# Performance work log

Measured on AMD Instinct MI355X. Metric: run time of the kernel, lower is better.

The kernel has to match this reference:

```python
import jax, jax.numpy as jnp
import numpy as np

N_USERS = 100000
N_ITEMS = 50000
N_NODES = N_USERS + N_ITEMS
EMB = 64
N_LAYERS = 3
N_EDGES = 4800000
AVG_DEG = 32


def setup_inputs() -> dict:
    key = jax.random.key(0)
    k1, k2, k3, k4, k5 = jax.random.split(key, 5)
    user_emb = jax.random.normal(k1, (N_USERS, EMB), dtype=jnp.float32) * 0.01
    item_emb = jax.random.normal(k2, (N_ITEMS, EMB), dtype=jnp.float32) * 0.01
    # normalized adjacency values ~ 1/deg
    adj_val = jax.random.uniform(k3, (N_EDGES,), dtype=jnp.float32) * (1.0 / AVG_DEG)
    adj_row = jax.random.randint(k4, (N_EDGES,), 0, N_NODES, dtype=jnp.int32)
    adj_col = jax.random.randint(k5, (N_EDGES,), 0, N_NODES, dtype=jnp.int32)
    return {"user_emb": user_emb, "item_emb": item_emb,
            "adj_val": adj_val, "adj_row": adj_row, "adj_col": adj_col}


def reference(user_emb, item_emb, adj_val, adj_row, adj_col):
    ego = jnp.concatenate([user_emb, item_emb], axis=0)  # [N_NODES, EMB]

    def spmm(x):
        # sparse_adj @ x via gather + segment-sum over destination rows
        msgs = adj_val[:, None] * x[adj_col]              # [N_EDGES, EMB]
        return jax.ops.segment_sum(msgs, adj_row, num_segments=N_NODES)

    acc = ego  # running sum for layer-mean (avoids stacking all layers)
    x = ego
    for _ in range(N_LAYERS):
        x = jax.nn.relu(spmm(x))
        acc = acc + x
    all_emb = acc / (N_LAYERS + 1)
    return all_emb[:N_USERS], all_emb[N_USERS:]
```

## Files before the change

### kernel.cpp

```cpp
#include <hip/hip_runtime.h>

#define N_USERS 100000
#define N_ITEMS 50000
#define N_NODES 150000
#define EMB 64
#define N_EDGES 4800000
#define N_LAYERS 3

#define RPB 128
#define NB 1172
#define MAXB 5120
#define CHUNK 8192
#define NCHUNKS ((N_EDGES + CHUNK - 1) / CHUNK)

__global__ __launch_bounds__(256) void init_kernel(
        const float2* __restrict__ user, const float2* __restrict__ item,
        unsigned short* __restrict__ x8, float* __restrict__ xs,
        float2* __restrict__ out) {
    int t = threadIdx.x;
    int p = t & 31;
    int r = blockIdx.x * 8 + (t >> 5);
    if (r >= N_NODES) return;
    float2 e = (r < N_USERS) ? user[r * 32 + p] : item[(r - N_USERS) * 32 + p];
    int o = r * 32 + p;
    out[o] = make_float2(0.25f * e.x, 0.25f * e.y);
    float m = fmaxf(fabsf(e.x), fabsf(e.y));
    #pragma unroll
    for (int mask = 16; mask; mask >>= 1) m = fmaxf(m, __shfl_xor(m, mask));
    float inv = (m > 0.f) ? 127.0f / m : 0.f;
    int q0 = (int)rintf(e.x * inv);
    int q1 = (int)rintf(e.y * inv);
    x8[o] = (unsigned short)((q0 & 0xFF) | ((q1 & 0xFF) << 8));
    if (p == 0) xs[r] = m * (1.0f / 127.0f);
}

__global__ __launch_bounds__(256) void hist_kernel(
        const int* __restrict__ row, int* __restrict__ counts) {
    __shared__ int h[NB];
    for (int i = threadIdx.x; i < NB; i += 256) h[i] = 0;
    __syncthreads();
    for (int i = blockIdx.x * 256 + threadIdx.x; i < N_EDGES; i += gridDim.x * 256)
        atomicAdd(&h[row[i] >> 7], 1);
    __syncthreads();
    for (int i = threadIdx.x; i < NB; i += 256) {
        int v = h[i];
        if (v) atomicAdd(&counts[i], v);
    }
}

__global__ __launch_bounds__(1024) void scan_kernel(
        const int* __restrict__ counts,
        int* __restrict__ bucketStart, int* __restrict__ cursor) {
    __shared__ int tmp[1024];
    int t = threadIdx.x;
    int i0 = 2 * t, i1 = 2 * t + 1;
    int v0 = (i0 < NB) ? counts[i0] : 0;
    int v1 = (i1 < NB) ? counts[i1] : 0;
    int s = v0 + v1;
    tmp[t] = s;
    __syncthreads();
    for (int off = 1; off < 1024; off <<= 1) {
        int u = (t >= off) ? tmp[t - off] : 0;
        __syncthreads();
        tmp[t] += u;
        __syncthreads();
    }
    int excl = tmp[t] - s;
    if (i0 < NB) { bucketStart[i0] = excl;      cursor[i0] = excl; }
    if (i1 < NB) { bucketStart[i1] = excl + v0; cursor[i1] = excl + v0; }
    if (t == 0) bucketStart[NB] = N_EDGES;
}

__global__ __launch_bounds__(512) void chunkscatter_kernel(
        const int* __restrict__ row, const int* __restrict__ col,
        const float* __restrict__ val,
        int* __restrict__ cursor, int2* __restrict__ sEdge) {
    __shared__ int2 rec[CHUNK];
    __shared__ unsigned short bidS[CHUNK];
    __shared__ int cnt[NB];
    __shared__ int lofs[NB];
    __shared__ int gbase[NB];
    __shared__ int tmp[512];

    int t = threadIdx.x;
    int e0 = blockIdx.x * CHUNK;
    int n = N_EDGES - e0; if (n > CHUNK) n = CHUNK;

    for (int i = t; i < NB; i += 512) cnt[i] = 0;
    __syncthreads();

    int2 myrec[16];
    int  myb[16];
    #pragma unroll
    for (int j = 0; j < 16; ++j) {
        int i = j * 512 + t;
        if (i < n) {
            int gi = e0 + i;
            int r = row[gi];
            int b = r >> 7;
            myrec[j] = make_int2(((r & (RPB - 1)) << 18) | col[gi],
                                 __float_as_int(val[gi]));
            myb[j] = b;
            atomicAdd(&cnt[b], 1);
        } else myb[j] = -1;
    }
    __syncthreads();

    int b3 = t * 3;
    int c0 = (b3     < NB) ? cnt[b3]     : 0;
    int c1 = (b3 + 1 < NB) ? cnt[b3 + 1] : 0;
    int c2 = (b3 + 2 < NB) ? cnt[b3 + 2] : 0;
    int s = c0 + c1 + c2;
    tmp[t] = s;
    __syncthreads();
    for (int off = 1; off < 512; off <<= 1) {
        int u = (t >= off) ? tmp[t - off] : 0;
        __syncthreads();
        tmp[t] += u;
        __syncthreads();
    }
    int excl = tmp[t] - s;
    if (b3     < NB) lofs[b3]     = excl;
    if (b3 + 1 < NB) lofs[b3 + 1] = excl + c0;
    if (b3 + 2 < NB) lofs[b3 + 2] = excl + c0 + c1;
    __syncthreads();

    for (int i = t; i < NB; i += 512) {
        int c = cnt[i];
        gbase[i] = c ? atomicAdd(&cursor[i], c) : 0;
        cnt[i] = lofs[i];
    }
    __syncthreads();

    #pragma unroll
    for (int j = 0; j < 16; ++j) {
        if (myb[j] >= 0) {
            int p = atomicAdd(&cnt[myb[j]], 1);
            rec[p] = myrec[j];
            bidS[p] = (unsigned short)myb[j];
        }
    }
    __syncthreads();

    for (int i = t; i < n; i += 512) {
        int b = bidS[i];
        sEdge[gbase[b] + (i - lofs[b])] = rec[i];
    }
}

__global__ __launch_bounds__(256) void localsort_kernel(
        const int* __restrict__ bucketStart, int2* __restrict__ sEdge,
        int* __restrict__ rowStart) {
    __shared__ int2 sorted[MAXB];
    __shared__ int lh[RPB];
    __shared__ int lsc[RPB];
    __shared__ int lcur[RPB];
    int b = blockIdx.x, t = threadIdx.x;
    int s0 = bucketStart[b];
    int s1 = bucketStart[b + 1];
    int size = s1 - s0;

    int2 e[20];
    #pragma unroll
    for (int j = 0; j < 20; ++j) {
        int idx = s0 + j * 256 + t;
        if (idx < s1) e[j] = sEdge[idx];
    }
    if (t < RPB) lh[t] = 0;
    __syncthreads();
    #pragma unroll
    for (int j = 0; j < 20; ++j) {
        int idx = s0 + j * 256 + t;
        if (idx < s1) atomicAdd(&lh[e[j].x >> 18], 1);
    }
    __syncthreads();
    if (t < RPB) lsc[t] = lh[t];
    __syncthreads();
    for (int off = 1; off < RPB; off <<= 1) {
        int u = 0;
        if (t < RPB && t >= off) u = lsc[t - off];
        __syncthreads();
        if (t < RPB) lsc[t] += u;
        __syncthreads();
    }
    if (t < RPB) {
        int excl = lsc[t] - lh[t];
        lcur[t] = excl;
        int node = b * RPB + t;
        if (node <= N_NODES) rowStart[node] = s0 + excl;
    }
    __syncthreads();
    #pragma unroll
    for (int j = 0; j < 20; ++j) {
        int idx = s0 + j * 256 + t;
        if (idx < s1) {
            int rl = e[j].x >> 18;
            int pos = atomicAdd(&lcur[rl], 1);
            sorted[pos] = make_int2(e[j].x & 0x3FFFF, e[j].y);
        }
    }
    __syncthreads();
    for (int j = t; j < size; j += 256) sEdge[s0 + j] = sorted[j];
}

__global__ __launch_bounds__(256, 4) void gather_kernel(
        const int* __restrict__ rowStart, const int2* __restrict__ sEdge,
        const unsigned short* __restrict__ x8, const float* __restrict__ xs,
        unsigned short* __restrict__ y8, float* __restrict__ ys,
        float2* __restrict__ out, int last) {
    __shared__ int2 eds[8][32];
    int t = threadIdx.x;
    int p = t & 31;
    int h = t >> 5;
    int r = blockIdx.x * 8 + h;
    if (r >= N_NODES) return;
    int start = rowStart[r];
    int end   = rowStart[r + 1];
    float2 acc = make_float2(0.f, 0.f);

    for (int base = start; base < end; base += 32) {
        int idx = base + p;
        int2 ed = (idx < end) ? sEdge[idx] : make_int2(0, 0);
        float w0 = __int_as_float(ed.y) * xs[ed.x];
        eds[h][p] = make_int2(ed.x, __float_as_int(w0));

        unsigned qv[32];
        float    wf[32];
        #pragma unroll
        for (int j = 0; j < 32; ++j) {
            int2 e = eds[h][j];
            wf[j] = __int_as_float(e.y);
            qv[j] = x8[e.x * 32 + p];
        }
        #pragma unroll
        for (int j = 0; j < 32; ++j) {
            acc.x = fmaf(wf[j], (float)(signed char)(qv[j] & 0xFF), acc.x);
            acc.y = fmaf(wf[j], (float)(signed char)(qv[j] >> 8), acc.y);
        }
    }

    float rx = fmaxf(acc.x, 0.f);
    float ry = fmaxf(acc.y, 0.f);
    int o = r * 32 + p;
    float2 ov = out[o];
    ov.x += 0.25f * rx; ov.y += 0.25f * ry;
    out[o] = ov;
    if (!last) {
        float m = fmaxf(rx, ry);
        #pragma unroll
        for (int mask = 16; mask; mask >>= 1) m = fmaxf(m, __shfl_xor(m, mask));
        float inv = (m > 0.f) ? 127.0f / m : 0.f;
        int q0 = (int)(rx * inv + 0.5f);
        int q1 = (int)(ry * inv + 0.5f);
        y8[o] = (unsigned short)(q0 | (q1 << 8));
        if (p == 0) ys[r] = m * (1.0f / 127.0f);
    }
}

extern "C" void kernel_launch(void* const* d_in, const int* in_sizes, int n_in,
                              void* d_out, int out_size, void* d_ws, size_t ws_size,
                              hipStream_t stream) {
    const float* user_emb = (const float*)d_in[0];
    const float* item_emb = (const float*)d_in[1];
    const float* adj_val  = (const float*)d_in[2];
    const int*   adj_row  = (const int*)d_in[3];
    const int*   adj_col  = (const int*)d_in[4];
    float* out = (float*)d_out;

    char* p = (char*)d_ws;
    int*  counts      = (int*)p;  p += ((size_t)NB * 4 + 15) & ~15ull;
    int*  bucketStart = (int*)p;  p += ((size_t)(NB + 1) * 4 + 15) & ~15ull;
    int*  cursor      = (int*)p;  p += ((size_t)NB * 4 + 15) & ~15ull;
    int*  rowStart    = (int*)p;  p += ((size_t)(N_NODES + 1) * 4 + 15) & ~15ull;
    int2* sEdge       = (int2*)p; p += (size_t)N_EDGES * 8;
    unsigned short* xq0 = (unsigned short*)p; p += (size_t)N_NODES * EMB;
    unsigned short* xq1 = (unsigned short*)p; p += (size_t)N_NODES * EMB;
    float* xsc0       = (float*)p; p += (size_t)N_NODES * 4;
    float* xsc1       = (float*)p;

    const int rowBlocks = (N_NODES + 7) / 8;

    init_kernel<<<rowBlocks, 256, 0, stream>>>(
        (const float2*)user_emb, (const float2*)item_emb,
        xq0, xsc0, (float2*)out);

    hipMemsetAsync(counts, 0, (size_t)NB * 4, stream);
    hist_kernel<<<512, 256, 0, stream>>>(adj_row, counts);
    scan_kernel<<<1, 1024, 0, stream>>>(counts, bucketStart, cursor);
    chunkscatter_kernel<<<NCHUNKS, 512, 0, stream>>>(
        adj_row, adj_col, adj_val, cursor, sEdge);
    localsort_kernel<<<NB, 256, 0, stream>>>(bucketStart, sEdge, rowStart);

    unsigned short* x = xq0; float* sx = xsc0;
    unsigned short* y = xq1; float* sy = xsc1;
    for (int l = 0; l < N_LAYERS; ++l) {
        gather_kernel<<<rowBlocks, 256, 0, stream>>>(
            rowStart, sEdge, x, sx, y, sy, (float2*)out, l == N_LAYERS - 1);
        unsigned short* tq = x; x = y; y = tq;
        float* ts = sx; sx = sy; sy = ts;
    }
}
```

Measured before the change: 567.1 us.

## Use unsigned biased int8 encoding and pre-shifted column offsets in gather

Layer-0 embeddings are now stored as unsigned bytes with a +128 bias. The bias is removed after accumulation by subtracting 128 times the summed weights. Later layers, which are non-negative after ReLU, use the full 0-255 range. Column indices are pre-shifted by 6 in the sorted edge list so the gather computes addresses without a multiply. The inner loop now runs only over valid 8-edge groups instead of all 32 slots, which skips padded loads for short rows but drops the separate load-then-FMA batching that kept 32 loads in flight.

```diff
diff --git a/kernel.cpp b/kernel.cpp
--- a/kernel.cpp
+++ b/kernel.cpp
@@ -28,9 +28,9 @@
     #pragma unroll
     for (int mask = 16; mask; mask >>= 1) m = fmaxf(m, __shfl_xor(m, mask));
     float inv = (m > 0.f) ? 127.0f / m : 0.f;
-    int q0 = (int)rintf(e.x * inv);
-    int q1 = (int)rintf(e.y * inv);
-    x8[o] = (unsigned short)((q0 & 0xFF) | ((q1 & 0xFF) << 8));
+    int q0 = (int)rintf(e.x * inv) + 128;
+    int q1 = (int)rintf(e.y * inv) + 128;
+    x8[o] = (unsigned short)(q0 | (q1 << 8));
     if (p == 0) xs[r] = m * (1.0f / 127.0f);
 }
 
@@ -196,13 +196,14 @@
         if (idx < s1) {
             int rl = e[j].x >> 18;
             int pos = atomicAdd(&lcur[rl], 1);
-            sorted[pos] = make_int2(e[j].x & 0x3FFFF, e[j].y);
+            sorted[pos] = make_int2((e[j].x & 0x3FFFF) << 6, e[j].y);
         }
     }
     __syncthreads();
     for (int j = t; j < size; j += 256) sEdge[s0 + j] = sorted[j];
 }
 
+template<int BIASED>
 __global__ __launch_bounds__(256, 4) void gather_kernel(
         const int* __restrict__ rowStart, const int2* __restrict__ sEdge,
         const unsigned short* __restrict__ x8, const float* __restrict__ xs,
@@ -217,26 +218,32 @@
     int start = rowStart[r];
     int end   = rowStart[r + 1];
     float2 acc = make_float2(0.f, 0.f);
+    float ws = 0.f;
+    const char* __restrict__ xp = (const char*)x8 + 2 * p;
 
     for (int base = start; base < end; base += 32) {
         int idx = base + p;
         int2 ed = (idx < end) ? sEdge[idx] : make_int2(0, 0);
-        float w0 = __int_as_float(ed.y) * xs[ed.x];
+        float w0 = __int_as_float(ed.y) * xs[ed.x >> 6];
         eds[h][p] = make_int2(ed.x, __float_as_int(w0));
 
-        unsigned qv[32];
-        float    wf[32];
-        #pragma unroll
-        for (int j = 0; j < 32; ++j) {
-            int2 e = eds[h][j];
-            wf[j] = __int_as_float(e.y);
-            qv[j] = x8[e.x * 32 + p];
+        int cnt = end - base; if (cnt > 32) cnt = 32;
+        int nb = (cnt + 7) >> 3;
+        for (int s8 = 0; s8 < nb; ++s8) {
+            #pragma unroll
+            for (int jj = 0; jj < 8; ++jj) {
+                int2 e = eds[h][s8 * 8 + jj];
+                float w = __int_as_float(e.y);
+                unsigned q = *(const unsigned short*)(xp + e.x);
+                acc.x = fmaf(w, (float)(q & 0xFFu), acc.x);
+                acc.y = fmaf(w, (float)((q >> 8) & 0xFFu), acc.y);
+                if (BIASED) ws += w;
+            }
         }
-        #pragma unroll
-        for (int j = 0; j < 32; ++j) {
-            acc.x = fmaf(wf[j], (float)(signed char)(qv[j] & 0xFF), acc.x);
-            acc.y = fmaf(wf[j], (float)(signed char)(qv[j] >> 8), acc.y);
-        }
+    }
+    if (BIASED) {
+        acc.x = fmaf(-128.f, ws, acc.x);
+        acc.y = fmaf(-128.f, ws, acc.y);
     }
 
     float rx = fmaxf(acc.x, 0.f);
@@ -249,11 +256,11 @@
         float m = fmaxf(rx, ry);
         #pragma unroll
         for (int mask = 16; mask; mask >>= 1) m = fmaxf(m, __shfl_xor(m, mask));
-        float inv = (m > 0.f) ? 127.0f / m : 0.f;
+        float inv = (m > 0.f) ? 255.0f / m : 0.f;
         int q0 = (int)(rx * inv + 0.5f);
         int q1 = (int)(ry * inv + 0.5f);
         y8[o] = (unsigned short)(q0 | (q1 << 8));
-        if (p == 0) ys[r] = m * (1.0f / 127.0f);
+        if (p == 0) ys[r] = m * (1.0f / 255.0f);
     }
 }
 
@@ -294,8 +301,12 @@
     unsigned short* x = xq0; float* sx = xsc0;
     unsigned short* y = xq1; float* sy = xsc1;
     for (int l = 0; l < N_LAYERS; ++l) {
-        gather_kernel<<<rowBlocks, 256, 0, stream>>>(
-            rowStart, sEdge, x, sx, y, sy, (float2*)out, l == N_LAYERS - 1);
+        if (l == 0)
+            gather_kernel<1><<<rowBlocks, 256, 0, stream>>>(
+                rowStart, sEdge, x, sx, y, sy, (float2*)out, 0);
+        else
+            gather_kernel<0><<<rowBlocks, 256, 0, stream>>>(
+                rowStart, sEdge, x, sx, y, sy, (float2*)out, l == N_LAYERS - 1);
         unsigned short* tq = x; x = y; y = tq;
         float* ts = sx; sx = sy; sy = ts;
     }
```

New measurement: 567.9 us. Within noise of the previous version (+0.1%).
